# Optimization experiments

Measured on AMD Instinct MI355X. Metric: run time of the kernel, lower is better.

## Reference

```python
import jax, jax.numpy as jnp
import numpy as np

D_MODEL = 1024
N_HEADS = 16
HEAD_DIM = D_MODEL // N_HEADS
D_FF = 4 * D_MODEL
EPS = 1e-5


def layer_norm(x, gamma, beta):
    mu = jnp.mean(x, axis=-1, keepdims=True)
    var = jnp.var(x, axis=-1, keepdims=True)
    return (x - mu) * jax.lax.rsqrt(var + EPS) * gamma + beta


def setup_inputs() -> dict:
    key = jax.random.key(0)
    ks = jax.random.split(key, 12)
    B, T, S = 4, 2048, 2048
    s_in = 1.0 / np.sqrt(D_MODEL)
    s_ff = 1.0 / np.sqrt(D_FF)
    return {
        "x": jax.random.normal(ks[0], (B, T, D_MODEL), jnp.float32),
        "context": jax.random.normal(ks[1], (B, S, D_MODEL), jnp.float32),
        "Wq": jax.random.normal(ks[2], (D_MODEL, D_MODEL), jnp.float32) * s_in,
        "Wk": jax.random.normal(ks[3], (D_MODEL, D_MODEL), jnp.float32) * s_in,
        "Wv": jax.random.normal(ks[4], (D_MODEL, D_MODEL), jnp.float32) * s_in,
        "Wo": jax.random.normal(ks[5], (D_MODEL, D_MODEL), jnp.float32) * s_in,
        "W1": jax.random.normal(ks[6], (D_FF, D_MODEL), jnp.float32) * s_in,
        "W2": jax.random.normal(ks[7], (D_MODEL, D_FF), jnp.float32) * s_ff,
        "g1": jnp.ones((D_MODEL,), jnp.float32),
        "b1": jnp.zeros((D_MODEL,), jnp.float32),
        "gc": jnp.ones((D_MODEL,), jnp.float32),
        "bc": jnp.zeros((D_MODEL,), jnp.float32),
        "g2": jnp.ones((D_MODEL,), jnp.float32),
        "b2": jnp.zeros((D_MODEL,), jnp.float32),
    }


def reference(x, context, Wq, Wk, Wv, Wo, W1, W2, g1, b1, gc, bc, g2, b2):
    B, T, C = x.shape
    S = context.shape[1]
    residual = x
    xn = layer_norm(x, g1, b1)
    cn = layer_norm(context, gc, bc)
    # torch Linear: y = x @ W.T ; split heads -> [B, H, T, Dh]
    q = (xn @ Wq.T).reshape(B, T, N_HEADS, HEAD_DIM).transpose(0, 2, 1, 3)
    k = (cn @ Wk.T).reshape(B, S, N_HEADS, HEAD_DIM).transpose(0, 2, 1, 3)
    v = (cn @ Wv.T).reshape(B, S, N_HEADS, HEAD_DIM).transpose(0, 2, 1, 3)
    scale = HEAD_DIM ** (-0.5)
    attn = jax.nn.softmax(jnp.einsum('bhtd,bhsd->bhts', q, k) * scale, axis=-1)
    o = jnp.einsum('bhts,bhsd->bhtd', attn, v).transpose(0, 2, 1, 3).reshape(B, T, C)
    x = residual + o @ Wo.T
    residual = x
    h = layer_norm(x, g2, b2)
    h = jax.nn.gelu(h @ W1.T, approximate=False) @ W2.T
    return residual + h
```

## Files before the change

### kernel.cpp

```cpp
#include <hip/hip_runtime.h>
#include <cstdint>
#include <cstddef>

typedef __attribute__((ext_vector_type(8))) short short8;
typedef __attribute__((ext_vector_type(4))) short short4v;
typedef __attribute__((ext_vector_type(4))) float f32x4;
typedef __attribute__((ext_vector_type(2))) unsigned uint2v;

#define DEV static __device__ __forceinline__

DEV short f2bf(float f) {
    unsigned u = __builtin_bit_cast(unsigned, f);
    unsigned r = (u + 0x7fffu + ((u >> 16) & 1u)) >> 16;
    return (short)r;
}

DEV unsigned cvt_pk_bf16(float a, float b) {
    unsigned r;
    asm("v_cvt_pk_bf16_f32 %0, %1, %2" : "=v"(r) : "v"(a), "v"(b));
    return r;
}

DEV float exp2_hw(float x) {
    float r;
    asm("v_exp_f32 %0, %1" : "=v"(r) : "v"(x));
    return r;
}

DEV void gld16(const void* g, void* l) {
    __builtin_amdgcn_global_load_lds((const __attribute__((address_space(1))) void*)g,
                                     (__attribute__((address_space(3))) void*)l, 16, 0, 0);
}

#define MFMA(c, a, b) asm volatile("v_mfma_f32_16x16x32_bf16 %0, %1, %2, %0" : "+v"(c) : "v"(a), "v"(b))

__global__ __launch_bounds__(256) void cvt_weights(
    const float* __restrict__ wq, const float* __restrict__ wk,
    const float* __restrict__ wv, const float* __restrict__ wo,
    const float* __restrict__ w1, const float* __restrict__ w2,
    short* __restrict__ dst) {
    long long gid = (long long)blockIdx.x * 256 + threadIdx.x;
    long long i4 = gid * 4;
    const float* src; long long loc;
    if (i4 < (4LL << 20)) {
        int s = (int)(i4 >> 20);
        src = (s == 0) ? wq : (s == 1) ? wk : (s == 2) ? wv : wo;
        loc = i4 & ((1LL << 20) - 1);
    } else {
        long long r = i4 - (4LL << 20);
        int s = (int)(r >> 22);
        src = s ? w2 : w1;
        loc = r & ((1LL << 22) - 1);
    }
    float4 v = *(const float4*)(src + loc);
    short4v o;
    o.x = f2bf(v.x); o.y = f2bf(v.y); o.z = f2bf(v.z); o.w = f2bf(v.w);
    *(short4v*)(dst + i4) = o;
}

__global__ __launch_bounds__(256) void ln_bf16(const float* __restrict__ x,
                                               const float* __restrict__ g,
                                               const float* __restrict__ bt,
                                               short* __restrict__ out) {
    int row = blockIdx.x;
    const float4* xr = (const float4*)(x + (size_t)row * 1024);
    float4 v = xr[threadIdx.x];
    float s  = v.x + v.y + v.z + v.w;
    float s2 = v.x*v.x + v.y*v.y + v.z*v.z + v.w*v.w;
    #pragma unroll
    for (int m = 1; m < 64; m <<= 1) { s += __shfl_xor(s, m); s2 += __shfl_xor(s2, m); }
    __shared__ float red[8];
    int wid = threadIdx.x >> 6;
    if ((threadIdx.x & 63) == 0) { red[wid] = s; red[4 + wid] = s2; }
    __syncthreads();
    s  = red[0] + red[1] + red[2] + red[3];
    s2 = red[4] + red[5] + red[6] + red[7];
    float mu  = s * (1.0f / 1024.0f);
    float var = fmaxf(s2 * (1.0f / 1024.0f) - mu * mu, 0.0f);
    float rs  = rsqrtf(var + 1e-5f);
    float4 gv = ((const float4*)g)[threadIdx.x];
    float4 bv = ((const float4*)bt)[threadIdx.x];
    short4v o;
    o.x = f2bf((v.x - mu) * rs * gv.x + bv.x);
    o.y = f2bf((v.y - mu) * rs * gv.y + bv.y);
    o.z = f2bf((v.z - mu) * rs * gv.z + bv.z);
    o.w = f2bf((v.w - mu) * rs * gv.w + bv.w);
    *(short4v*)(out + (size_t)row * 1024 + (size_t)threadIdx.x * 4) = o;
}

template<int MODE>
__global__ __launch_bounds__(256) void gemm_bt(const short* __restrict__ A,
                                               const short* __restrict__ B,
                                               void* __restrict__ out,
                                               const float* __restrict__ resid,
                                               int M, int N, int K, float osc) {
    __shared__ short lA[2][128 * 32];
    __shared__ short lB[2][128 * 32];
    int tid = threadIdx.x;
    int nbn = N >> 7;
    int bm = blockIdx.x / nbn, bn = blockIdx.x % nbn;
    int row0 = bm << 7, col0 = bn << 7;
    int wid = tid >> 6, lane = tid & 63;
    int wm = wid >> 1, wn = wid & 1;
    int lr = lane & 15, lg = lane >> 4;

    f32x4 acc[4][4] = {};

    auto stage = [&](int buf, int kst) {
        const short* Ab = A + (size_t)row0 * K + kst * 32;
        const short* Bb = B + (size_t)col0 * K + kst * 32;
        #pragma unroll
        for (int c = 0; c < 2; ++c) {
            int idx = c * 256 + tid;
            int r = idx >> 2, sp = idx & 3;
            int sl = sp ^ ((r >> 1) & 3);
            gld16(Ab + (size_t)r * K + sl * 8, &lA[buf][idx * 8]);
            gld16(Bb + (size_t)r * K + sl * 8, &lB[buf][idx * 8]);
        }
    };

    int NK = K >> 5;
    stage(0, 0);
    __syncthreads();
    for (int ks = 0; ks < NK; ++ks) {
        int cur = ks & 1;
        if (ks + 1 < NK) stage(cur ^ 1, ks + 1);
        const short* pa = lA[cur];
        const short* pb = lB[cur];
        short8 af[4], bf[4];
        #pragma unroll
        for (int f = 0; f < 4; ++f) {
            int ra = wm * 64 + f * 16 + lr;
            af[f] = *(const short8*)(pa + ra * 32 + ((lg ^ ((ra >> 1) & 3)) << 3));
            int rb = wn * 64 + f * 16 + lr;
            bf[f] = *(const short8*)(pb + rb * 32 + ((lg ^ ((rb >> 1) & 3)) << 3));
        }
        #pragma unroll
        for (int i = 0; i < 4; ++i)
            #pragma unroll
            for (int j = 0; j < 4; ++j)
                MFMA(acc[i][j], af[i], bf[j]);
        __syncthreads();
    }
    asm volatile("s_nop 7\n\ts_nop 7");

    int orow0 = row0 + wm * 64, ocol0 = col0 + wn * 64;
    #pragma unroll
    for (int i = 0; i < 4; ++i)
        #pragma unroll
        for (int j = 0; j < 4; ++j)
            #pragma unroll
            for (int r = 0; r < 4; ++r) {
                int gr = orow0 + i * 16 + lg * 4 + r;
                int gc = ocol0 + j * 16 + lr;
                size_t off = (size_t)gr * N + gc;
                float v = acc[i][j][r];
                if constexpr (MODE == 0) {
                    ((short*)out)[off] = f2bf(v);
                } else if constexpr (MODE == 1) {
                    ((float*)out)[off] = v + resid[off];
                } else if constexpr (MODE == 2) {
                    float t = 0.5f * v * (1.0f + erff(v * 0.70710678118f));
                    ((short*)out)[off] = f2bf(t);
                } else {
                    ((short*)out)[off] = f2bf(v * osc);
                }
            }
}

__global__ __launch_bounds__(256) void attn(const short* __restrict__ Q,
                                            const short* __restrict__ K,
                                            const short* __restrict__ Vt,
                                            short* __restrict__ O) {
    __shared__ short lK[64 * 64];
    __shared__ short lV[64 * 64];
    __shared__ short lP[4][32 * 64];
    int tid = threadIdx.x;
    int qt = blockIdx.x & 15;
    int bh = blockIdx.x >> 4;
    int b = bh >> 4, h = bh & 15;
    int wid = tid >> 6, lane = tid & 63;
    int lr = lane & 15, lg = lane >> 4;
    int q0 = qt * 128 + wid * 32;

    short8 qf[2][2];
    #pragma unroll
    for (int fm = 0; fm < 2; ++fm)
        #pragma unroll
        for (int kb = 0; kb < 2; ++kb) {
            size_t roff = (size_t)(b * 2048 + q0 + fm * 16 + lr) * 1024 + h * 64 + kb * 32 + lg * 8;
            qf[fm][kb] = *(const short8*)(Q + roff);
        }

    f32x4 oacc[2][4] = {};
    float mrow[2] = { -1e30f, -1e30f };
    float lrs[2]  = { 0.0f, 0.0f };

    const short* Kb = K + (size_t)(b * 2048) * 1024 + h * 64;
    const short* Vb = Vt + (size_t)(h * 64) * 8192 + b * 2048;
    short* Pw = lP[wid];
    int albase = (lane & 48) >> 2;

    for (int st = 0; st < 32; ++st) {
        #pragma unroll
        for (int c = 0; c < 2; ++c) {
            int idx = c * 256 + tid;
            int r = idx >> 3, sp = idx & 7;
            int sl = sp ^ (r & 7);
            gld16(Kb + (size_t)(st * 64 + r) * 1024 + sl * 8, &lK[idx * 8]);
            gld16(Vb + (size_t)r * 8192 + st * 64 + sl * 8, &lV[idx * 8]);
        }
        __syncthreads();

        f32x4 sc2[4][2] = {};
        #pragma unroll
        for (int kb = 0; kb < 2; ++kb) {
            short8 kf[4];
            #pragma unroll
            for (int fn = 0; fn < 4; ++fn) {
                int kr = fn * 16 + lr;
                kf[fn] = *(const short8*)(lK + kr * 64 + (((kb * 4 + lg) ^ (kr & 7)) << 3));
            }
            #pragma unroll
            for (int fn = 0; fn < 4; ++fn)
                #pragma unroll
                for (int fm = 0; fm < 2; ++fm)
                    MFMA(sc2[fn][fm], kf[fn], qf[fm][kb]);
        }
        asm volatile("s_nop 7\n\ts_nop 7");

        #pragma unroll
        for (int fm = 0; fm < 2; ++fm) {
            float pm = sc2[0][fm][0];
            #pragma unroll
            for (int fn = 0; fn < 4; ++fn)
                #pragma unroll
                for (int r = 0; r < 4; ++r)
                    if (fn | r) pm = fmaxf(pm, sc2[fn][fm][r]);
            pm = fmaxf(pm, __shfl_xor(pm, 16));
            pm = fmaxf(pm, __shfl_xor(pm, 32));

            float mo = mrow[fm];
            float mn = mo;
            float al = 1.0f;
            if (!__all(pm <= mo + 8.0f)) {
                mn = fmaxf(mo, pm);
                al = exp2_hw(mo - mn);
                mrow[fm] = mn;
                #pragma unroll
                for (int r = 0; r < 4; ++r) {
                    float alr = __shfl(al, albase + r);
                    #pragma unroll
                    for (int fn = 0; fn < 4; ++fn) oacc[fm][fn][r] *= alr;
                }
            }

            float p[4][4];
            float ps = 0.0f;
            #pragma unroll
            for (int fn = 0; fn < 4; ++fn)
                #pragma unroll
                for (int r = 0; r < 4; ++r) {
                    p[fn][r] = exp2_hw(sc2[fn][fm][r] - mn);
                    ps += p[fn][r];
                }
            ps += __shfl_xor(ps, 16);
            ps += __shfl_xor(ps, 32);
            lrs[fm] = lrs[fm] * al + ps;

            int pr = fm * 16 + lr;
            int swz = (pr & 7) << 3;
            #pragma unroll
            for (int fn = 0; fn < 4; ++fn) {
                uint2v w;
                w.x = cvt_pk_bf16(p[fn][0], p[fn][1]);
                w.y = cvt_pk_bf16(p[fn][2], p[fn][3]);
                *(uint2v*)(Pw + ((pr * 64 + fn * 16 + lg * 4) ^ swz)) = w;
            }
        }

        #pragma unroll
        for (int kb = 0; kb < 2; ++kb) {
            short8 pa[2], vf[4];
            #pragma unroll
            for (int fm = 0; fm < 2; ++fm) {
                int pr = fm * 16 + lr;
                pa[fm] = *(const short8*)(Pw + pr * 64 + (((kb * 4 + lg) ^ (pr & 7)) << 3));
            }
            #pragma unroll
            for (int fn = 0; fn < 4; ++fn) {
                int vr = fn * 16 + lr;
                vf[fn] = *(const short8*)(lV + vr * 64 + (((kb * 4 + lg) ^ (vr & 7)) << 3));
            }
            #pragma unroll
            for (int fm = 0; fm < 2; ++fm)
                #pragma unroll
                for (int fn = 0; fn < 4; ++fn)
                    MFMA(oacc[fm][fn], pa[fm], vf[fn]);
        }
        __syncthreads();
    }
    asm volatile("s_nop 7\n\ts_nop 7");

    #pragma unroll
    for (int fm = 0; fm < 2; ++fm)
        #pragma unroll
        for (int r = 0; r < 4; ++r) {
            float linv = __shfl(lrs[fm], albase + r);
            float inv = 1.0f / linv;
            #pragma unroll
            for (int fn = 0; fn < 4; ++fn) {
                size_t off = (size_t)(b * 2048 + q0 + fm * 16 + lg * 4 + r) * 1024 + h * 64 + fn * 16 + lr;
                O[off] = f2bf(oacc[fm][fn][r] * inv);
            }
        }
}

extern "C" void kernel_launch(void* const* d_in, const int* in_sizes, int n_in,
                              void* d_out, int out_size, void* d_ws, size_t ws_size,
                              hipStream_t stream) {
    const float* x   = (const float*)d_in[0];
    const float* ctx = (const float*)d_in[1];
    const float* Wq  = (const float*)d_in[2];
    const float* Wk  = (const float*)d_in[3];
    const float* Wv  = (const float*)d_in[4];
    const float* Wo  = (const float*)d_in[5];
    const float* W1  = (const float*)d_in[6];
    const float* W2  = (const float*)d_in[7];
    const float* g1  = (const float*)d_in[8];
    const float* b1  = (const float*)d_in[9];
    const float* gc  = (const float*)d_in[10];
    const float* bc  = (const float*)d_in[11];
    const float* g2  = (const float*)d_in[12];
    const float* b2  = (const float*)d_in[13];

    char* ws = (char*)d_ws;
    const size_t OFF_W  = 0;
    const size_t OFF_XN = 25165824;
    const size_t OFF_CN = OFF_XN + 16777216;
    const size_t OFF_QB = OFF_CN + 16777216;
    const size_t OFF_KB = OFF_QB + 16777216;
    const size_t OFF_VT = OFF_KB + 16777216;
    const size_t OFF_X2 = OFF_VT + 16777216;
    const size_t OFF_F1 = OFF_X2 + 33554432;

    short* Wb = (short*)(ws + OFF_W);
    short* XN = (short*)(ws + OFF_XN);
    short* CN = (short*)(ws + OFF_CN);
    short* QB = (short*)(ws + OFF_QB);
    short* KB = (short*)(ws + OFF_KB);
    short* VT = (short*)(ws + OFF_VT);
    float* X2 = (float*)(ws + OFF_X2);
    short* F1 = (short*)(ws + OFF_F1);
    short* OB = XN;
    short* H  = CN;

    const size_t WQo = 0, WKo = 1048576, WVo = 2097152, WOo = 3145728;
    const size_t W1o = 4194304, W2o = 8388608;
    const float QSCALE = 0.125f * 1.4426950408889634f;

    cvt_weights<<<12288, 256, 0, stream>>>(Wq, Wk, Wv, Wo, W1, W2, Wb);
    ln_bf16<<<8192, 256, 0, stream>>>(x, g1, b1, XN);
    ln_bf16<<<8192, 256, 0, stream>>>(ctx, gc, bc, CN);
    gemm_bt<3><<<512, 256, 0, stream>>>(XN, Wb + WQo, QB, nullptr, 8192, 1024, 1024, QSCALE);
    gemm_bt<0><<<512, 256, 0, stream>>>(CN, Wb + WKo, KB, nullptr, 8192, 1024, 1024, 1.0f);
    gemm_bt<0><<<512, 256, 0, stream>>>(Wb + WVo, CN, VT, nullptr, 1024, 8192, 1024, 1.0f);
    attn<<<1024, 256, 0, stream>>>(QB, KB, VT, OB);
    gemm_bt<1><<<512, 256, 0, stream>>>(OB, Wb + WOo, X2, x, 8192, 1024, 1024, 1.0f);
    ln_bf16<<<8192, 256, 0, stream>>>(X2, g2, b2, H);
    gemm_bt<2><<<2048, 256, 0, stream>>>(H, Wb + W1o, F1, nullptr, 8192, 4096, 1024, 1.0f);
    gemm_bt<1><<<512, 256, 0, stream>>>(F1, Wb + W2o, (float*)d_out, X2, 8192, 1024, 4096, 1.0f);
}
```

Measured before the change: 490.1 us.

## Replace GEMM with 256x128 tiles, triple-buffered LDS pipeline and grid swizzle

```diff
diff --git a/kernel.cpp b/kernel.cpp
--- a/kernel.cpp
+++ b/kernel.cpp
@@ -33,6 +33,7 @@
 }
 
 #define MFMA(c, a, b) asm volatile("v_mfma_f32_16x16x32_bf16 %0, %1, %2, %0" : "+v"(c) : "v"(a), "v"(b))
+#define BAR() asm volatile("s_barrier" ::: "memory")
 
 __global__ __launch_bounds__(256) void cvt_weights(
     const float* __restrict__ wq, const float* __restrict__ wk,
@@ -89,64 +90,89 @@
 }
 
 template<int MODE>
-__global__ __launch_bounds__(256) void gemm_bt(const short* __restrict__ A,
-                                               const short* __restrict__ B,
-                                               void* __restrict__ out,
-                                               const float* __restrict__ resid,
-                                               int M, int N, int K, float osc) {
-    __shared__ short lA[2][128 * 32];
-    __shared__ short lB[2][128 * 32];
-    int tid = threadIdx.x;
-    int nbn = N >> 7;
-    int bm = blockIdx.x / nbn, bn = blockIdx.x % nbn;
-    int row0 = bm << 7, col0 = bn << 7;
-    int wid = tid >> 6, lane = tid & 63;
-    int wm = wid >> 1, wn = wid & 1;
-    int lr = lane & 15, lg = lane >> 4;
-
-    f32x4 acc[4][4] = {};
-
-    auto stage = [&](int buf, int kst) {
-        const short* Ab = A + (size_t)row0 * K + kst * 32;
-        const short* Bb = B + (size_t)col0 * K + kst * 32;
-        #pragma unroll
-        for (int c = 0; c < 2; ++c) {
-            int idx = c * 256 + tid;
-            int r = idx >> 2, sp = idx & 3;
-            int sl = sp ^ ((r >> 1) & 3);
-            gld16(Ab + (size_t)r * K + sl * 8, &lA[buf][idx * 8]);
-            gld16(Bb + (size_t)r * K + sl * 8, &lB[buf][idx * 8]);
+__global__ __launch_bounds__(256, 2) void gemm8(const short* __restrict__ A,
+                                                const short* __restrict__ B,
+                                                void* __restrict__ out,
+                                                const float* __restrict__ resid,
+                                                int M, int N, int K, float osc) {
+    __shared__ short lds[3 * 12288];
+    const int tid = threadIdx.x;
+    const int nbn = N >> 7;
+    int cpx = gridDim.x >> 3;
+    int swz = (blockIdx.x & 7) * cpx + (blockIdx.x >> 3);
+    int bm = swz / nbn, bn = swz % nbn;
+    const int row0 = bm << 8, col0 = bn << 7;
+    const int wid = tid >> 6, lane = tid & 63;
+    const int wm = wid >> 1, wn = wid & 1;
+    const int lr = lane & 15, lg = lane >> 4;
+
+    auto stage = [&](int kt, int bb, int h) {
+        const short* Ab = A + (size_t)row0 * K + kt * 32;
+        const short* Bb = B + (size_t)col0 * K + kt * 32;
+        #pragma unroll
+        for (int l = 0; l < 2; ++l) {
+            int g = (h * 2 + l) * 256 + tid;
+            int r = g >> 2;
+            int sl = (g & 3) ^ ((r >> 1) & 3);
+            gld16(Ab + (size_t)r * K + sl * 8, &lds[bb + g * 8]);
+        }
+        {
+            int g = h * 256 + tid;
+            int r = g >> 2;
+            int sl = (g & 3) ^ ((r >> 1) & 3);
+            gld16(Bb + (size_t)r * K + sl * 8, &lds[bb + 8192 + g * 8]);
         }
     };
 
-    int NK = K >> 5;
-    stage(0, 0);
-    __syncthreads();
-    for (int ks = 0; ks < NK; ++ks) {
-        int cur = ks & 1;
-        if (ks + 1 < NK) stage(cur ^ 1, ks + 1);
-        const short* pa = lA[cur];
-        const short* pb = lB[cur];
-        short8 af[4], bf[4];
-        #pragma unroll
-        for (int f = 0; f < 4; ++f) {
-            int ra = wm * 64 + f * 16 + lr;
-            af[f] = *(const short8*)(pa + ra * 32 + ((lg ^ ((ra >> 1) & 3)) << 3));
-            int rb = wn * 64 + f * 16 + lr;
-            bf[f] = *(const short8*)(pb + rb * 32 + ((lg ^ ((rb >> 1) & 3)) << 3));
-        }
-        #pragma unroll
-        for (int i = 0; i < 4; ++i)
-            #pragma unroll
-            for (int j = 0; j < 4; ++j)
-                MFMA(acc[i][j], af[i], bf[j]);
-        __syncthreads();
+    f32x4 acc[8][4] = {};
+    const int NK = K >> 5;
+
+    stage(0, 0, 0);     stage(0, 0, 1);
+    stage(1, 12288, 0); stage(1, 12288, 1);
+    asm volatile("s_waitcnt vmcnt(6)" ::: "memory");
+    BAR();
+
+    int cb = 0, sb = 2;
+    const int rsw = ((lr >> 1) & 3);
+    short8 bfr[4];
+    for (int kt = 0; kt < NK; ++kt) {
+        int bb = cb * 12288, sbb = sb * 12288;
+        bool st = (kt + 2) < NK;
+        #pragma unroll
+        for (int p = 0; p < 2; ++p) {
+            short8 af[4];
+            int csw = (lg ^ rsw) << 3;
+            #pragma unroll
+            for (int i = 0; i < 4; ++i)
+                af[i] = *(const short8*)(lds + bb + (wm * 128 + (p * 4 + i) * 16 + lr) * 32 + csw);
+            if (p == 0) {
+                #pragma unroll
+                for (int j = 0; j < 4; ++j)
+                    bfr[j] = *(const short8*)(lds + bb + 8192 + (wn * 64 + j * 16 + lr) * 32 + csw);
+            }
+            if (st) stage(kt + 2, sbb, p);
+            BAR();
+            __builtin_amdgcn_s_setprio(1);
+            #pragma unroll
+            for (int i = 0; i < 4; ++i)
+                #pragma unroll
+                for (int j = 0; j < 4; ++j)
+                    MFMA(acc[p * 4 + i][j], af[i], bfr[j]);
+            __builtin_amdgcn_s_setprio(0);
+            if (p == 1) {
+                if (st) asm volatile("s_waitcnt vmcnt(6)" ::: "memory");
+                else    asm volatile("s_waitcnt vmcnt(0)" ::: "memory");
+            }
+            BAR();
+        }
+        cb = (cb == 2) ? 0 : cb + 1;
+        sb = (sb == 2) ? 0 : sb + 1;
     }
     asm volatile("s_nop 7\n\ts_nop 7");
 
-    int orow0 = row0 + wm * 64, ocol0 = col0 + wn * 64;
+    int orow0 = row0 + wm * 128, ocol0 = col0 + wn * 64;
     #pragma unroll
-    for (int i = 0; i < 4; ++i)
+    for (int i = 0; i < 8; ++i)
         #pragma unroll
         for (int j = 0; j < 4; ++j)
             #pragma unroll
@@ -362,12 +388,12 @@
     cvt_weights<<<12288, 256, 0, stream>>>(Wq, Wk, Wv, Wo, W1, W2, Wb);
     ln_bf16<<<8192, 256, 0, stream>>>(x, g1, b1, XN);
     ln_bf16<<<8192, 256, 0, stream>>>(ctx, gc, bc, CN);
-    gemm_bt<3><<<512, 256, 0, stream>>>(XN, Wb + WQo, QB, nullptr, 8192, 1024, 1024, QSCALE);
-    gemm_bt<0><<<512, 256, 0, stream>>>(CN, Wb + WKo, KB, nullptr, 8192, 1024, 1024, 1.0f);
-    gemm_bt<0><<<512, 256, 0, stream>>>(Wb + WVo, CN, VT, nullptr, 1024, 8192, 1024, 1.0f);
+    gemm8<3><<<256, 256, 0, stream>>>(XN, Wb + WQo, QB, nullptr, 8192, 1024, 1024, QSCALE);
+    gemm8<0><<<256, 256, 0, stream>>>(CN, Wb + WKo, KB, nullptr, 8192, 1024, 1024, 1.0f);
+    gemm8<0><<<256, 256, 0, stream>>>(Wb + WVo, CN, VT, nullptr, 1024, 8192, 1024, 1.0f);
     attn<<<1024, 256, 0, stream>>>(QB, KB, VT, OB);
-    gemm_bt<1><<<512, 256, 0, stream>>>(OB, Wb + WOo, X2, x, 8192, 1024, 1024, 1.0f);
+    gemm8<1><<<256, 256, 0, stream>>>(OB, Wb + WOo, X2, x, 8192, 1024, 1024, 1.0f);
     ln_bf16<<<8192, 256, 0, stream>>>(X2, g2, b2, H);
-    gemm_bt<2><<<2048, 256, 0, stream>>>(H, Wb + W1o, F1, nullptr, 8192, 4096, 1024, 1.0f);
-    gemm_bt<1><<<512, 256, 0, stream>>>(F1, Wb + W2o, (float*)d_out, X2, 8192, 1024, 4096, 1.0f);
-}
+    gemm8<2><<<1024, 256, 0, stream>>>(H, Wb + W1o, F1, nullptr, 8192, 4096, 1024, 1.0f);
+    gemm8<1><<<256, 256, 0, stream>>>(F1, Wb + W2o, (float*)d_out, X2, 8192, 1024, 4096, 1.0f);
+}
```

New measurement: 474.8 us. -3.1%, faster.
